# Optimization experiments

Hardware: AMD Instinct MI355X
Metric: run time of the kernel (lower is better)

The kernel has to match this reference:

```python
import jax, jax.numpy as jnp
import numpy as np

N_NODES = 100000


def _degrees(src, dst):
    ones = jnp.ones(src.shape[0], dtype=jnp.float32)
    out_deg = jax.ops.segment_sum(ones, src, num_segments=N_NODES)
    in_deg = jax.ops.segment_sum(ones, dst, num_segments=N_NODES)
    # DGL clamps degrees to a minimum of 1 before the power
    inv_sqrt_out = jax.lax.rsqrt(jnp.maximum(out_deg, 1.0))
    inv_sqrt_in = jax.lax.rsqrt(jnp.maximum(in_deg, 1.0))
    return inv_sqrt_out, inv_sqrt_in


def _graph_conv(h, W, b, src, dst, inv_sqrt_out, inv_sqrt_in):
    # DGL GraphConv, norm='both': D_out^{-1/2} on src feats, SpMM-sum, D_in^{-1/2} on dst
    h = h * inv_sqrt_out[:, None]
    h = h @ W  # applying weight before aggregation is mathematically identical
    agg = jax.ops.segment_sum(h[src], dst, num_segments=N_NODES)
    return agg * inv_sqrt_in[:, None] + b


def setup_inputs() -> dict:
    key = jax.random.key(0)
    ks = jax.random.split(key, 6)
    E, IN, HID = 1600000, 128, 128
    scale = 1.0 / np.sqrt(IN)
    return {
        "feat": jax.random.normal(ks[0], (N_NODES, IN), dtype=jnp.float32),
        "W0": jax.random.normal(ks[1], (IN, HID), dtype=jnp.float32) * scale,
        "b0": jnp.zeros((HID,), dtype=jnp.float32),
        "W1": jax.random.normal(ks[2], (HID, HID), dtype=jnp.float32) * scale,
        "b1": jnp.zeros((HID,), dtype=jnp.float32),
        "W2": jax.random.normal(ks[3], (HID, HID), dtype=jnp.float32) * scale,
        "b2": jnp.zeros((HID,), dtype=jnp.float32),
        "src": jax.random.randint(ks[4], (E,), 0, N_NODES, dtype=jnp.int32),
        "dst": jax.random.randint(ks[5], (E,), 0, N_NODES, dtype=jnp.int32),
    }


def reference(feat, W0, b0, W1, b1, W2, b2, src, dst):
    inv_sqrt_out, inv_sqrt_in = _degrees(src, dst)
    skips = [feat]
    h = feat
    for W, b in ((W0, b0), (W1, b1), (W2, b2)):
        h = jax.nn.relu(_graph_conv(h, W, b, src, dst, inv_sqrt_out, inv_sqrt_in))
        skips.append(h)
    return jnp.concatenate(skips, axis=1)  # torch.hstack on 2D == concat along dim 1
```

## Files before the change

### kernel.cpp

```cpp
#include <hip/hip_runtime.h>
#include <hip/hip_fp16.h>

#define NN 100000
#define NE 1600000
#define FD 128
#define OS 512
#define LDA 136
#define NBKT 196
#define PCH 4096

typedef __attribute__((ext_vector_type(8))) short short8;
typedef __attribute__((ext_vector_type(4))) float f32x4;

struct h4v { __half2 lo, hi; };

__device__ __forceinline__ short f2bf(float x) {
    unsigned u = __float_as_uint(x);
    u = (u + 0x7fff + ((u >> 16) & 1)) >> 16;
    return (short)u;
}

__global__ void k_init_out(const float* __restrict__ feat, float* __restrict__ out) {
    const size_t total = (size_t)NN * 32;
    for (size_t i = (size_t)blockIdx.x * blockDim.x + threadIdx.x; i < total;
         i += (size_t)gridDim.x * blockDim.x) {
        size_t n = i >> 5;
        int c4 = (int)(i & 31);
        ((float4*)(out + n * OS))[c4] = ((const float4*)feat)[n * 32 + c4];
    }
}

__global__ void k_prep_w(const float* __restrict__ W0, const float* __restrict__ W1,
                         const float* __restrict__ W2, short* __restrict__ Wt) {
    int i = blockIdx.x * blockDim.x + threadIdx.x;
    if (i >= 3 * FD * FD) return;
    int l = i >> 14, r = i & (FD * FD - 1);
    int n = r >> 7, k = r & 127;
    const float* W = (l == 0) ? W0 : ((l == 1) ? W1 : W2);
    Wt[i] = f2bf(W[k * FD + n]);
}

__global__ __launch_bounds__(256) void k_deg(const int* __restrict__ src,
                                             const int* __restrict__ dst,
                                             int* __restrict__ cnt_out,
                                             int* __restrict__ bktcnt) {
    __shared__ int h[NBKT];
    for (int i = threadIdx.x; i < NBKT; i += 256) h[i] = 0;
    __syncthreads();
    const int total4 = NE / 4;
    for (int i = blockIdx.x * blockDim.x + threadIdx.x; i < total4;
         i += gridDim.x * blockDim.x) {
        int4 s = ((const int4*)src)[i];
        int4 d = ((const int4*)dst)[i];
        atomicAdd(&cnt_out[s.x], 1); atomicAdd(&cnt_out[s.y], 1);
        atomicAdd(&cnt_out[s.z], 1); atomicAdd(&cnt_out[s.w], 1);
        atomicAdd(&h[d.x >> 9], 1); atomicAdd(&h[d.y >> 9], 1);
        atomicAdd(&h[d.z >> 9], 1); atomicAdd(&h[d.w >> 9], 1);
    }
    __syncthreads();
    for (int i = threadIdx.x; i < NBKT; i += 256)
        if (h[i]) atomicAdd(&bktcnt[i], h[i]);
}

__global__ void k_invsqrt(const int* __restrict__ cnt, float* __restrict__ inv, int n) {
    int i = blockIdx.x * blockDim.x + threadIdx.x;
    if (i < n) inv[i] = rsqrtf((float)max(cnt[i], 1));
}

__global__ __launch_bounds__(256) void k_bkt_scan(const int* __restrict__ bktcnt,
                                                  int* __restrict__ bkt_base,
                                                  int* __restrict__ bkt_cursor) {
    __shared__ int s[256];
    const int tid = threadIdx.x;
    int v = (tid < NBKT) ? bktcnt[tid] : 0;
    s[tid] = v;
    __syncthreads();
    for (int off = 1; off < 256; off <<= 1) {
        int t = (tid >= off) ? s[tid - off] : 0;
        __syncthreads();
        s[tid] += t;
        __syncthreads();
    }
    int excl = s[tid] - v;
    if (tid < NBKT) { bkt_base[tid] = excl; bkt_cursor[tid] = excl; }
    if (tid == NBKT - 1) bkt_base[NBKT] = excl + v;
}

__global__ __launch_bounds__(256) void k_part(const int* __restrict__ src,
                                              const int* __restrict__ dst,
                                              int* __restrict__ bkt_cursor,
                                              int2* __restrict__ pairs) {
    __shared__ int hist[NBKT];
    __shared__ int base[NBKT];
    __shared__ int lofs[NBKT];
    const int tid = threadIdx.x;
    const int e0 = blockIdx.x * PCH;
    for (int i = tid; i < NBKT; i += 256) { hist[i] = 0; lofs[i] = 0; }
    __syncthreads();
    int md[16], ms[16];
    #pragma unroll
    for (int k = 0; k < 16; ++k) {
        int e = e0 + k * 256 + tid;
        md[k] = (e < NE) ? dst[e] : -1;
        ms[k] = (e < NE) ? src[e] : 0;
    }
    #pragma unroll
    for (int k = 0; k < 16; ++k)
        if (md[k] >= 0) atomicAdd(&hist[md[k] >> 9], 1);
    __syncthreads();
    for (int i = tid; i < NBKT; i += 256)
        base[i] = hist[i] ? atomicAdd(&bkt_cursor[i], hist[i]) : 0;
    __syncthreads();
    #pragma unroll
    for (int k = 0; k < 16; ++k)
        if (md[k] >= 0) {
            int b = md[k] >> 9;
            int off = atomicAdd(&lofs[b], 1);
            pairs[base[b] + off] = make_int2(ms[k], md[k]);
        }
}

__global__ __launch_bounds__(256) void k_build(const int2* __restrict__ pairs,
                                               const int* __restrict__ bkt_base,
                                               int* __restrict__ row_ptr,
                                               int* __restrict__ col,
                                               float* __restrict__ inv_in) {
    __shared__ int cnt_s[512];
    __shared__ int wsum[4];
    const int b = blockIdx.x;
    const int tid = threadIdx.x;
    const int lane = tid & 63, wid = tid >> 6;
    const int ebeg = bkt_base[b], eend = bkt_base[b + 1];
    const int n0 = b << 9;
    cnt_s[tid] = 0; cnt_s[tid + 256] = 0;
    __syncthreads();
    for (int e = ebeg + tid; e < eend; e += 256)
        atomicAdd(&cnt_s[pairs[e].y - n0], 1);
    __syncthreads();
    const int v0 = cnt_s[2 * tid], v1 = cnt_s[2 * tid + 1];
    const int sum2 = v0 + v1;
    int incl = sum2;
    #pragma unroll
    for (int off = 1; off < 64; off <<= 1) {
        int t = __shfl_up(incl, off, 64);
        if (lane >= off) incl += t;
    }
    if (lane == 63) wsum[wid] = incl;
    __syncthreads();
    if (tid == 0) {
        int c = 0;
        #pragma unroll
        for (int i = 0; i < 4; ++i) { int t = wsum[i]; wsum[i] = c; c += t; }
    }
    __syncthreads();
    const int e0 = wsum[wid] + incl - sum2;
    cnt_s[2 * tid] = e0;
    cnt_s[2 * tid + 1] = e0 + v0;
    const int g0 = n0 + 2 * tid, g1 = g0 + 1;
    if (g0 < NN) { row_ptr[g0] = ebeg + e0; inv_in[g0] = rsqrtf((float)max(v0, 1)); }
    if (g1 < NN) { row_ptr[g1] = ebeg + e0 + v0; inv_in[g1] = rsqrtf((float)max(v1, 1)); }
    if (b == NBKT - 1 && tid == 0) row_ptr[NN] = eend;
    __syncthreads();
    for (int e = ebeg + tid; e < eend; e += 256) {
        int2 p = pairs[e];
        int pos = atomicAdd(&cnt_s[p.y - n0], 1);
        col[ebeg + pos] = p.x;
    }
}

__global__ __launch_bounds__(256) void k_gemm(const float* __restrict__ h, int hstride,
                                              const short* __restrict__ Wt,
                                              const float* __restrict__ inv_out,
                                              __half* __restrict__ tmp) {
    __shared__ short Ws[FD * LDA];
    __shared__ short hA[64 * LDA];
    const int tid = threadIdx.x;
    for (int i = tid; i < FD * 16; i += 256) {
        int n = i >> 4, c = i & 15;
        short8 v = *(const short8*)(Wt + n * FD + c * 8);
        *(short8*)(&Ws[n * LDA + c * 8]) = v;
    }
    const int row0 = blockIdx.x * 128;
    const int wid = tid >> 6, lane = tid & 63;
    const int m = lane & 15, quad = lane >> 4;

    for (int sub = 0; sub < 2; ++sub) {
        const int rbase = row0 + sub * 64;
        __syncthreads();
        for (int i = tid; i < 64 * 32; i += 256) {
            int r = i >> 5, c4 = i & 31;
            int gr = rbase + r;
            float4 v = make_float4(0.f, 0.f, 0.f, 0.f);
            if (gr < NN) v = ((const float4*)(h + (size_t)gr * hstride))[c4];
            short4 b;
            b.x = f2bf(v.x); b.y = f2bf(v.y); b.z = f2bf(v.z); b.w = f2bf(v.w);
            *(short4*)(&hA[r * LDA + c4 * 4]) = b;
        }
        __syncthreads();
        const int rtile = rbase + wid * 16;
        short8 a0 = *(const short8*)(&hA[(wid * 16 + m) * LDA + 0 * 32 + quad * 8]);
        short8 a1 = *(const short8*)(&hA[(wid * 16 + m) * LDA + 1 * 32 + quad * 8]);
        short8 a2 = *(const short8*)(&hA[(wid * 16 + m) * LDA + 2 * 32 + quad * 8]);
        short8 a3 = *(const short8*)(&hA[(wid * 16 + m) * LDA + 3 * 32 + quad * 8]);
        float s0, s1, s2, s3;
        {
            int r = rtile + quad * 4;
            s0 = (r + 0 < NN) ? inv_out[r + 0] : 0.f;
            s1 = (r + 1 < NN) ? inv_out[r + 1] : 0.f;
            s2 = (r + 2 < NN) ? inv_out[r + 2] : 0.f;
            s3 = (r + 3 < NN) ? inv_out[r + 3] : 0.f;
        }
        #pragma unroll
        for (int ct = 0; ct < 8; ++ct) {
            f32x4 acc = {0.f, 0.f, 0.f, 0.f};
            short8 b0 = *(const short8*)(&Ws[(ct * 16 + m) * LDA + 0 * 32 + quad * 8]);
            short8 b1 = *(const short8*)(&Ws[(ct * 16 + m) * LDA + 1 * 32 + quad * 8]);
            short8 b2 = *(const short8*)(&Ws[(ct * 16 + m) * LDA + 2 * 32 + quad * 8]);
            short8 b3 = *(const short8*)(&Ws[(ct * 16 + m) * LDA + 3 * 32 + quad * 8]);
            acc = __builtin_amdgcn_mfma_f32_16x16x32_bf16(a0, b0, acc, 0, 0, 0);
            acc = __builtin_amdgcn_mfma_f32_16x16x32_bf16(a1, b1, acc, 0, 0, 0);
            acc = __builtin_amdgcn_mfma_f32_16x16x32_bf16(a2, b2, acc, 0, 0, 0);
            acc = __builtin_amdgcn_mfma_f32_16x16x32_bf16(a3, b3, acc, 0, 0, 0);
            const int r = rtile + quad * 4;
            const int c = ct * 16 + m;
            if (r + 3 < NN) {
                tmp[(size_t)(r + 0) * FD + c] = __float2half_rn(acc[0] * s0);
                tmp[(size_t)(r + 1) * FD + c] = __float2half_rn(acc[1] * s1);
                tmp[(size_t)(r + 2) * FD + c] = __float2half_rn(acc[2] * s2);
                tmp[(size_t)(r + 3) * FD + c] = __float2half_rn(acc[3] * s3);
            } else {
                if (r + 0 < NN) tmp[(size_t)(r + 0) * FD + c] = __float2half_rn(acc[0] * s0);
                if (r + 1 < NN) tmp[(size_t)(r + 1) * FD + c] = __float2half_rn(acc[1] * s1);
                if (r + 2 < NN) tmp[(size_t)(r + 2) * FD + c] = __float2half_rn(acc[2] * s2);
                if (r + 3 < NN) tmp[(size_t)(r + 3) * FD + c] = __float2half_rn(acc[3] * s3);
            }
        }
    }
}

__global__ __launch_bounds__(256) void k_gather(const __half* __restrict__ tmp,
                                                const int* __restrict__ row_ptr,
                                                const int* __restrict__ col,
                                                const float* __restrict__ inv_in,
                                                const float* __restrict__ b,
                                                float* __restrict__ out, int off) {
    const int wid = threadIdx.x >> 6;
    const int lane = threadIdx.x & 63;
    const int half = lane >> 5;
    const int sl = lane & 31;
    const int node = blockIdx.x * 4 + wid;
    if (node >= NN) return;
    const int beg = row_ptr[node], end = row_ptr[node + 1];
    const h4v* t4 = (const h4v*)tmp;
    float4 acc = make_float4(0.f, 0.f, 0.f, 0.f);
    int j = beg + half;
    for (; j + 6 < end; j += 8) {
        int s0 = col[j], s1 = col[j + 2], s2 = col[j + 4], s3 = col[j + 6];
        h4v v0 = t4[(size_t)s0 * 32 + sl];
        h4v v1 = t4[(size_t)s1 * 32 + sl];
        h4v v2 = t4[(size_t)s2 * 32 + sl];
        h4v v3 = t4[(size_t)s3 * 32 + sl];
        float2 l0 = __half22float2(v0.lo), h0 = __half22float2(v0.hi);
        float2 l1 = __half22float2(v1.lo), h1 = __half22float2(v1.hi);
        float2 l2 = __half22float2(v2.lo), h2 = __half22float2(v2.hi);
        float2 l3 = __half22float2(v3.lo), h3 = __half22float2(v3.hi);
        acc.x += (l0.x + l1.x) + (l2.x + l3.x);
        acc.y += (l0.y + l1.y) + (l2.y + l3.y);
        acc.z += (h0.x + h1.x) + (h2.x + h3.x);
        acc.w += (h0.y + h1.y) + (h2.y + h3.y);
    }
    for (; j < end; j += 2) {
        h4v v = t4[(size_t)col[j] * 32 + sl];
        float2 l = __half22float2(v.lo), h = __half22float2(v.hi);
        acc.x += l.x; acc.y += l.y; acc.z += h.x; acc.w += h.y;
    }
    acc.x += __shfl_xor(acc.x, 32);
    acc.y += __shfl_xor(acc.y, 32);
    acc.z += __shfl_xor(acc.z, 32);
    acc.w += __shfl_xor(acc.w, 32);
    if (half == 0) {
        const float s = inv_in[node];
        const float4 bb = ((const float4*)b)[sl];
        float4 r;
        r.x = fmaxf(acc.x * s + bb.x, 0.f);
        r.y = fmaxf(acc.y * s + bb.y, 0.f);
        r.z = fmaxf(acc.z * s + bb.z, 0.f);
        r.w = fmaxf(acc.w * s + bb.w, 0.f);
        ((float4*)(out + (size_t)node * OS + off))[sl] = r;
    }
}

extern "C" void kernel_launch(void* const* d_in, const int* in_sizes, int n_in,
                              void* d_out, int out_size, void* d_ws, size_t ws_size,
                              hipStream_t stream) {
    const float* feat = (const float*)d_in[0];
    const float* W0 = (const float*)d_in[1];
    const float* b0 = (const float*)d_in[2];
    const float* W1 = (const float*)d_in[3];
    const float* b1 = (const float*)d_in[4];
    const float* W2 = (const float*)d_in[5];
    const float* b2 = (const float*)d_in[6];
    const int* src = (const int*)d_in[7];
    const int* dst = (const int*)d_in[8];
    float* out = (float*)d_out;
    float* ws = (float*)d_ws;

    __half* tmp = (__half*)ws;
    int2* pairs = (int2*)(ws + (size_t)NN * 64);
    float* base2 = ws + (size_t)NN * 128;
    int* cnt_out = (int*)base2;
    int* bktcnt = cnt_out + NN;
    int* bkt_base = bktcnt + NBKT;
    int* bkt_cursor = bkt_base + NBKT + 1;
    float* inv = (float*)(bkt_cursor + NBKT);
    int* row_ptr = (int*)(inv + 2 * NN);
    int* col = row_ptr + NN + 1;
    short* Wt = (short*)(col + NE);

    hipMemsetAsync(cnt_out, 0, (NN + NBKT) * sizeof(int), stream);
    k_init_out<<<4096, 256, 0, stream>>>(feat, out);
    k_prep_w<<<(3 * FD * FD + 255) / 256, 256, 0, stream>>>(W0, W1, W2, Wt);
    k_deg<<<2048, 256, 0, stream>>>(src, dst, cnt_out, bktcnt);
    k_bkt_scan<<<1, 256, 0, stream>>>(bktcnt, bkt_base, bkt_cursor);
    k_part<<<(NE + PCH - 1) / PCH, 256, 0, stream>>>(src, dst, bkt_cursor, pairs);
    k_build<<<NBKT, 256, 0, stream>>>(pairs, bkt_base, row_ptr, col, inv + NN);
    k_invsqrt<<<(NN + 255) / 256, 256, 0, stream>>>(cnt_out, inv, NN);

    const float* bs[3] = {b0, b1, b2};
    const float* h = feat;
    int hstride = FD;
    for (int l = 0; l < 3; ++l) {
        k_gemm<<<(NN + 127) / 128, 256, 0, stream>>>(h, hstride, Wt + l * FD * FD, inv, tmp);
        k_gather<<<(NN + 3) / 4, 256, 0, stream>>>(tmp, row_ptr, col, inv + NN, bs[l], out,
                                                   FD * (l + 1));
        h = out + FD * (l + 1);
        hstride = OS;
    }
}
```

Before: 669.3 us.

## Quantize transformed node features to int8 with per-row scales for gather

The GEMM output is now stored as int8 with a per-row absmax scale instead of fp16, halving the bytes each gathered neighbour row costs in the memory-bound SpMM aggregation. Each row is packed in a permuted column order so every lane writes one 8-byte word, and the gather undoes that permutation when writing output columns. This adds a per-edge scale load and extra multiplies, scatters the final stores, and loses precision, which may break the accuracy tolerance.

```diff
diff --git a/kernel.cpp b/kernel.cpp
--- a/kernel.cpp
+++ b/kernel.cpp
@@ -11,8 +11,6 @@
 
 typedef __attribute__((ext_vector_type(8))) short short8;
 typedef __attribute__((ext_vector_type(4))) float f32x4;
-
-struct h4v { __half2 lo, hi; };
 
 __device__ __forceinline__ short f2bf(float x) {
     unsigned u = __float_as_uint(x);
@@ -171,7 +169,8 @@
 __global__ __launch_bounds__(256) void k_gemm(const float* __restrict__ h, int hstride,
                                               const short* __restrict__ Wt,
                                               const float* __restrict__ inv_out,
-                                              __half* __restrict__ tmp) {
+                                              unsigned char* __restrict__ tmp8,
+                                              float* __restrict__ scales) {
     __shared__ short Ws[FD * LDA];
     __shared__ short hA[64 * LDA];
     const int tid = threadIdx.x;
@@ -210,6 +209,7 @@
             s2 = (r + 2 < NN) ? inv_out[r + 2] : 0.f;
             s3 = (r + 3 < NN) ? inv_out[r + 3] : 0.f;
         }
+        f32x4 accs[8];
         #pragma unroll
         for (int ct = 0; ct < 8; ++ct) {
             f32x4 acc = {0.f, 0.f, 0.f, 0.f};
@@ -221,28 +221,74 @@
             acc = __builtin_amdgcn_mfma_f32_16x16x32_bf16(a1, b1, acc, 0, 0, 0);
             acc = __builtin_amdgcn_mfma_f32_16x16x32_bf16(a2, b2, acc, 0, 0, 0);
             acc = __builtin_amdgcn_mfma_f32_16x16x32_bf16(a3, b3, acc, 0, 0, 0);
-            const int r = rtile + quad * 4;
-            const int c = ct * 16 + m;
+            acc[0] *= s0; acc[1] *= s1; acc[2] *= s2; acc[3] *= s3;
+            accs[ct] = acc;
+        }
+        float pm0 = 0.f, pm1 = 0.f, pm2 = 0.f, pm3 = 0.f;
+        #pragma unroll
+        for (int ct = 0; ct < 8; ++ct) {
+            pm0 = fmaxf(pm0, fabsf(accs[ct][0]));
+            pm1 = fmaxf(pm1, fabsf(accs[ct][1]));
+            pm2 = fmaxf(pm2, fabsf(accs[ct][2]));
+            pm3 = fmaxf(pm3, fabsf(accs[ct][3]));
+        }
+        #pragma unroll
+        for (int off = 1; off < 16; off <<= 1) {
+            pm0 = fmaxf(pm0, __shfl_xor(pm0, off));
+            pm1 = fmaxf(pm1, __shfl_xor(pm1, off));
+            pm2 = fmaxf(pm2, __shfl_xor(pm2, off));
+            pm3 = fmaxf(pm3, __shfl_xor(pm3, off));
+        }
+        const float is0 = pm0 > 0.f ? 127.f / pm0 : 0.f;
+        const float is1 = pm1 > 0.f ? 127.f / pm1 : 0.f;
+        const float is2 = pm2 > 0.f ? 127.f / pm2 : 0.f;
+        const float is3 = pm3 > 0.f ? 127.f / pm3 : 0.f;
+        const int r = rtile + quad * 4;
+        if (m == 0) {
+            const float inv127 = 1.f / 127.f;
             if (r + 3 < NN) {
-                tmp[(size_t)(r + 0) * FD + c] = __float2half_rn(acc[0] * s0);
-                tmp[(size_t)(r + 1) * FD + c] = __float2half_rn(acc[1] * s1);
-                tmp[(size_t)(r + 2) * FD + c] = __float2half_rn(acc[2] * s2);
-                tmp[(size_t)(r + 3) * FD + c] = __float2half_rn(acc[3] * s3);
+                float4 sv = make_float4(pm0 * inv127, pm1 * inv127, pm2 * inv127, pm3 * inv127);
+                *((float4*)(scales + r)) = sv;
             } else {
-                if (r + 0 < NN) tmp[(size_t)(r + 0) * FD + c] = __float2half_rn(acc[0] * s0);
-                if (r + 1 < NN) tmp[(size_t)(r + 1) * FD + c] = __float2half_rn(acc[1] * s1);
-                if (r + 2 < NN) tmp[(size_t)(r + 2) * FD + c] = __float2half_rn(acc[2] * s2);
-                if (r + 3 < NN) tmp[(size_t)(r + 3) * FD + c] = __float2half_rn(acc[3] * s3);
+                if (r + 0 < NN) scales[r + 0] = pm0 * inv127;
+                if (r + 1 < NN) scales[r + 1] = pm1 * inv127;
+                if (r + 2 < NN) scales[r + 2] = pm2 * inv127;
+                if (r + 3 < NN) scales[r + 3] = pm3 * inv127;
             }
         }
-    }
-}
-
-__global__ __launch_bounds__(256) void k_gather(const __half* __restrict__ tmp,
+        unsigned long long w0 = 0ull, w1 = 0ull, w2 = 0ull, w3 = 0ull;
+        #pragma unroll
+        for (int ct = 0; ct < 8; ++ct) {
+            unsigned char q0 = (unsigned char)(char)(int)rintf(accs[ct][0] * is0);
+            unsigned char q1 = (unsigned char)(char)(int)rintf(accs[ct][1] * is1);
+            unsigned char q2 = (unsigned char)(char)(int)rintf(accs[ct][2] * is2);
+            unsigned char q3 = (unsigned char)(char)(int)rintf(accs[ct][3] * is3);
+            w0 |= (unsigned long long)q0 << (8 * ct);
+            w1 |= (unsigned long long)q1 << (8 * ct);
+            w2 |= (unsigned long long)q2 << (8 * ct);
+            w3 |= (unsigned long long)q3 << (8 * ct);
+        }
+        unsigned char* base = tmp8 + (size_t)r * FD + m * 8;
+        if (r + 3 < NN) {
+            *(unsigned long long*)(base + 0 * FD) = w0;
+            *(unsigned long long*)(base + 1 * FD) = w1;
+            *(unsigned long long*)(base + 2 * FD) = w2;
+            *(unsigned long long*)(base + 3 * FD) = w3;
+        } else {
+            if (r + 0 < NN) *(unsigned long long*)(base + 0 * FD) = w0;
+            if (r + 1 < NN) *(unsigned long long*)(base + 1 * FD) = w1;
+            if (r + 2 < NN) *(unsigned long long*)(base + 2 * FD) = w2;
+            if (r + 3 < NN) *(unsigned long long*)(base + 3 * FD) = w3;
+        }
+    }
+}
+
+__global__ __launch_bounds__(256) void k_gather(const unsigned char* __restrict__ tmp8,
+                                                const float* __restrict__ scales,
                                                 const int* __restrict__ row_ptr,
                                                 const int* __restrict__ col,
                                                 const float* __restrict__ inv_in,
-                                                const float* __restrict__ b,
+                                                const float* __restrict__ bias,
                                                 float* __restrict__ out, int off) {
     const int wid = threadIdx.x >> 6;
     const int lane = threadIdx.x & 63;
@@ -251,42 +297,43 @@
     const int node = blockIdx.x * 4 + wid;
     if (node >= NN) return;
     const int beg = row_ptr[node], end = row_ptr[node + 1];
-    const h4v* t4 = (const h4v*)tmp;
-    float4 acc = make_float4(0.f, 0.f, 0.f, 0.f);
+    float a0 = 0.f, a1 = 0.f, a2 = 0.f, a3 = 0.f;
     int j = beg + half;
     for (; j + 6 < end; j += 8) {
         int s0 = col[j], s1 = col[j + 2], s2 = col[j + 4], s3 = col[j + 6];
-        h4v v0 = t4[(size_t)s0 * 32 + sl];
-        h4v v1 = t4[(size_t)s1 * 32 + sl];
-        h4v v2 = t4[(size_t)s2 * 32 + sl];
-        h4v v3 = t4[(size_t)s3 * 32 + sl];
-        float2 l0 = __half22float2(v0.lo), h0 = __half22float2(v0.hi);
-        float2 l1 = __half22float2(v1.lo), h1 = __half22float2(v1.hi);
-        float2 l2 = __half22float2(v2.lo), h2 = __half22float2(v2.hi);
-        float2 l3 = __half22float2(v3.lo), h3 = __half22float2(v3.hi);
-        acc.x += (l0.x + l1.x) + (l2.x + l3.x);
-        acc.y += (l0.y + l1.y) + (l2.y + l3.y);
-        acc.z += (h0.x + h1.x) + (h2.x + h3.x);
-        acc.w += (h0.y + h1.y) + (h2.y + h3.y);
+        char4 c0 = *(const char4*)(tmp8 + (size_t)s0 * FD + sl * 4);
+        char4 c1 = *(const char4*)(tmp8 + (size_t)s1 * FD + sl * 4);
+        char4 c2 = *(const char4*)(tmp8 + (size_t)s2 * FD + sl * 4);
+        char4 c3 = *(const char4*)(tmp8 + (size_t)s3 * FD + sl * 4);
+        float f0 = scales[s0], f1 = scales[s1], f2 = scales[s2], f3 = scales[s3];
+        a0 += f0 * (float)c0.x + f1 * (float)c1.x + f2 * (float)c2.x + f3 * (float)c3.x;
+        a1 += f0 * (float)c0.y + f1 * (float)c1.y + f2 * (float)c2.y + f3 * (float)c3.y;
+        a2 += f0 * (float)c0.z + f1 * (float)c1.z + f2 * (float)c2.z + f3 * (float)c3.z;
+        a3 += f0 * (float)c0.w + f1 * (float)c1.w + f2 * (float)c2.w + f3 * (float)c3.w;
     }
     for (; j < end; j += 2) {
-        h4v v = t4[(size_t)col[j] * 32 + sl];
-        float2 l = __half22float2(v.lo), h = __half22float2(v.hi);
-        acc.x += l.x; acc.y += l.y; acc.z += h.x; acc.w += h.y;
-    }
-    acc.x += __shfl_xor(acc.x, 32);
-    acc.y += __shfl_xor(acc.y, 32);
-    acc.z += __shfl_xor(acc.z, 32);
-    acc.w += __shfl_xor(acc.w, 32);
+        int s0 = col[j];
+        char4 c0 = *(const char4*)(tmp8 + (size_t)s0 * FD + sl * 4);
+        float f0 = scales[s0];
+        a0 += f0 * (float)c0.x;
+        a1 += f0 * (float)c0.y;
+        a2 += f0 * (float)c0.z;
+        a3 += f0 * (float)c0.w;
+    }
+    a0 += __shfl_xor(a0, 32);
+    a1 += __shfl_xor(a1, 32);
+    a2 += __shfl_xor(a2, 32);
+    a3 += __shfl_xor(a3, 32);
     if (half == 0) {
         const float s = inv_in[node];
-        const float4 bb = ((const float4*)b)[sl];
-        float4 r;
-        r.x = fmaxf(acc.x * s + bb.x, 0.f);
-        r.y = fmaxf(acc.y * s + bb.y, 0.f);
-        r.z = fmaxf(acc.z * s + bb.z, 0.f);
-        r.w = fmaxf(acc.w * s + bb.w, 0.f);
-        ((float4*)(out + (size_t)node * OS + off))[sl] = r;
+        float* ob = out + (size_t)node * OS + off;
+        float av[4] = {a0, a1, a2, a3};
+        #pragma unroll
+        for (int k = 0; k < 4; ++k) {
+            int jj = 4 * sl + k;
+            int c = ((jj & 7) << 4) + (jj >> 3);
+            ob[c] = fmaxf(av[k] * s + bias[c], 0.f);
+        }
     }
 }
 
@@ -305,8 +352,9 @@
     float* out = (float*)d_out;
     float* ws = (float*)d_ws;
 
-    __half* tmp = (__half*)ws;
+    unsigned char* tmp8 = (unsigned char*)ws;
     int2* pairs = (int2*)(ws + (size_t)NN * 64);
+    float* scales = ws + (size_t)NN * 96;
     float* base2 = ws + (size_t)NN * 128;
     int* cnt_out = (int*)base2;
     int* bktcnt = cnt_out + NN;
@@ -330,9 +378,10 @@
     const float* h = feat;
     int hstride = FD;
     for (int l = 0; l < 3; ++l) {
-        k_gemm<<<(NN + 127) / 128, 256, 0, stream>>>(h, hstride, Wt + l * FD * FD, inv, tmp);
-        k_gather<<<(NN + 3) / 4, 256, 0, stream>>>(tmp, row_ptr, col, inv + NN, bs[l], out,
-                                                   FD * (l + 1));
+        k_gemm<<<(NN + 127) / 128, 256, 0, stream>>>(h, hstride, Wt + l * FD * FD, inv,
+                                                     tmp8, scales);
+        k_gather<<<(NN + 3) / 4, 256, 0, stream>>>(tmp8, scales, row_ptr, col, inv + NN,
+                                                   bs[l], out, FD * (l + 1));
         h = out + FD * (l + 1);
         hstride = OS;
     }
```

Result: faster. 626.6 us (-6.4%).
